# Kernel optimization log

Hardware: AMD Instinct MI355X
Metric: run time of the kernel (lower is better)

The kernel has to match this reference:

```python
import jax, jax.numpy as jnp
import numpy as np

HEAD_NUM = 4
EMB = 128
N_NODES = 50000
N_EDGES = 600000


def setup_inputs() -> dict:
    key = jax.random.key(0)
    k1, k2, k3, k4, k5, k6 = jax.random.split(key, 6)
    embeds = jax.random.normal(k1, (N_NODES, EMB), dtype=jnp.float32)
    qW = jax.random.normal(k2, (EMB, EMB), dtype=jnp.float32) * (1.0 / np.sqrt(EMB))
    kW = jax.random.normal(k3, (EMB, EMB), dtype=jnp.float32) * (1.0 / np.sqrt(EMB))
    vW = jax.random.normal(k4, (EMB, EMB), dtype=jnp.float32) * (1.0 / np.sqrt(EMB))
    rows = jax.random.randint(k5, (N_EDGES,), 0, N_NODES, dtype=jnp.int32)
    cols = jax.random.randint(k6, (N_EDGES,), 0, N_NODES, dtype=jnp.int32)
    return {"embeds": embeds, "qW": qW, "kW": kW, "vW": vW,
            "rows": rows, "cols": cols, "n_nodes": N_NODES}


def reference(embeds, qW, kW, vW, rows, cols, n_nodes):
    H = HEAD_NUM
    D = embeds.shape[1]
    Dh = D // H
    rowEmb = embeds[rows]                                   # [E, D] gather
    colEmb = embeds[cols]                                   # [E, D] gather
    q = (rowEmb @ qW).reshape(-1, H, Dh)                    # [E, H, Dh]
    k = (colEmb @ kW).reshape(-1, H, Dh)
    v = (colEmb @ vW).reshape(-1, H, Dh)
    att = jnp.einsum('ehd,ehd->eh', q, k)                   # per-edge per-head logits
    att = jnp.clip(att, -10.0, 10.0)
    expAtt = jnp.exp(att)                                   # [E, H]
    attNorm = jax.ops.segment_sum(expAtt, rows, num_segments=n_nodes)  # [N, H]
    att = expAtt / (attNorm[rows] + 1e-8)                   # segment softmax
    res = (att[..., None] * v).reshape(-1, D)               # [E, D]
    out = jax.ops.segment_sum(res, rows, num_segments=n_nodes)  # [N, D]
    return out
```

## Files before the change

### kernel.cpp

```cpp
#include <hip/hip_runtime.h>
#include <math.h>

#define EMB 128
#define HEADS 4
#define ROWSTRIDE 152
#define OSTRIDE 260
#define CAP 64

typedef __attribute__((ext_vector_type(8))) _Float16 f16x8;
typedef __attribute__((ext_vector_type(4))) _Float16 f16x4;
typedef __attribute__((ext_vector_type(4))) float f32x4;

__global__ __launch_bounds__(256) void prep_w(
    const float* __restrict__ Wq, const float* __restrict__ Wk, const float* __restrict__ Wv,
    _Float16* __restrict__ Wfrag)
{
    int flat = blockIdx.x * 256 + threadIdx.x;
    int m    = flat >> 14;
    int rem  = flat & 16383;
    int ct   = rem >> 11;
    int s    = (rem >> 9) & 3;
    int lane = (rem >> 3) & 63;
    int j    = rem & 7;
    int k = s * 32 + (lane >> 4) * 8 + j;
    int n = ct * 16 + (lane & 15);
    const float* Ws[3] = { Wq, Wk, Wv };
    Wfrag[flat] = (_Float16)Ws[m][k * 128 + n];
}

__global__ __launch_bounds__(256) void mega_kernel(
    const float* __restrict__ embeds,
    const _Float16* __restrict__ Wfrag,
    _Float16* __restrict__ Qh, _Float16* __restrict__ KV,
    const int* __restrict__ rows, const int* __restrict__ cols,
    int* __restrict__ deg, int* __restrict__ slots,
    int N, int E, int PB)
{
    __shared__ __align__(16) _Float16 sBuf[64 * OSTRIDE];

    if (blockIdx.x >= PB) {
        int e = (blockIdx.x - PB) * 256 + threadIdx.x;
        if (e < E) {
            int r = rows[e];
            int pos = atomicAdd(&deg[r], 1);
            if (pos < CAP) slots[(size_t)r * CAP + pos] = cols[e];
        }
        return;
    }

    const int n0 = blockIdx.x * 64;
    const int t  = threadIdx.x;

    #pragma unroll
    for (int j = 0; j < 8; j++) {
        int flat = t + j * 256;
        int row  = flat >> 5;
        int c4   = flat & 31;
        int gn   = n0 + row;
        float4 v = (gn < N) ? reinterpret_cast<const float4*>(embeds)[(size_t)gn * 32 + c4]
                            : make_float4(0.f, 0.f, 0.f, 0.f);
        f16x4 u = { (_Float16)v.x, (_Float16)v.y, (_Float16)v.z, (_Float16)v.w };
        *reinterpret_cast<f16x4*>(&sBuf[row * ROWSTRIDE + c4 * 4]) = u;
    }
    __syncthreads();

    const int w    = t >> 6;
    const int lane = t & 63;
    const int nlo  = lane & 15;
    const int quad = lane >> 4;

    f16x8 a[4];
    #pragma unroll
    for (int s = 0; s < 4; s++) {
        int row = 16 * w + nlo;
        int k   = s * 32 + quad * 8;
        a[s] = *reinterpret_cast<const f16x8*>(&sBuf[row * ROWSTRIDE + k]);
    }
    __syncthreads();

    const int rowL = 16 * w + quad * 4;

    #pragma unroll
    for (int ct = 0; ct < 8; ct++) {
        f32x4 acc = { 0.f, 0.f, 0.f, 0.f };
        #pragma unroll
        for (int s = 0; s < 4; s++) {
            f16x8 b = *reinterpret_cast<const f16x8*>(
                Wfrag + ((size_t)(ct * 4 + s) * 64 + lane) * 8);
            acc = __builtin_amdgcn_mfma_f32_16x16x32_f16(a[s], b, acc, 0, 0, 0);
        }
        int col = ct * 16 + nlo;
        #pragma unroll
        for (int r = 0; r < 4; r++)
            sBuf[(rowL + r) * OSTRIDE + col] = (_Float16)acc[r];
    }
    __syncthreads();
    #pragma unroll
    for (int j = 0; j < 4; j++) {
        int flat = j * 2048 + t * 8;
        int row  = flat >> 7;
        int col  = flat & 127;
        int gn   = n0 + row;
        if (gn < N) {
            f16x8 v = *reinterpret_cast<const f16x8*>(&sBuf[row * OSTRIDE + col]);
            *reinterpret_cast<f16x8*>(&Qh[(size_t)gn * EMB + col]) = v;
        }
    }
    __syncthreads();

    #pragma unroll
    for (int m = 1; m < 3; m++) {
        int voff = (m == 2) ? 4 : 0;
        #pragma unroll
        for (int ct = 0; ct < 8; ct++) {
            f32x4 acc = { 0.f, 0.f, 0.f, 0.f };
            #pragma unroll
            for (int s = 0; s < 4; s++) {
                f16x8 b = *reinterpret_cast<const f16x8*>(
                    Wfrag + ((size_t)((m * 8 + ct) * 4 + s) * 64 + lane) * 8);
                acc = __builtin_amdgcn_mfma_f32_16x16x32_f16(a[s], b, acc, 0, 0, 0);
            }
            int col  = ct * 16 + nlo;
            int lidx = 8 * (col >> 2) + (col & 3) + voff;
            #pragma unroll
            for (int r = 0; r < 4; r++)
                sBuf[(rowL + r) * OSTRIDE + lidx] = (_Float16)acc[r];
        }
    }
    __syncthreads();
    #pragma unroll
    for (int j = 0; j < 8; j++) {
        int flat = j * 2048 + t * 8;
        int row  = flat >> 8;
        int col  = flat & 255;
        int gn   = n0 + row;
        if (gn < N) {
            f16x8 v = *reinterpret_cast<const f16x8*>(&sBuf[row * OSTRIDE + col]);
            *reinterpret_cast<f16x8*>(&KV[(size_t)gn * 256 + col]) = v;
        }
    }
}

__global__ __launch_bounds__(256) void node_fused(
    const _Float16* __restrict__ Qh, const _Float16* __restrict__ KV,
    const int* __restrict__ deg, const int* __restrict__ slots,
    float* __restrict__ out, int N)
{
    int n = blockIdx.x * 8 + (threadIdx.x >> 5);
    if (n >= N) return;
    int lane = threadIdx.x & 31;

    f16x4 qh = *reinterpret_cast<const f16x4*>(Qh + (size_t)n * EMB + lane * 4);
    float qx = (float)qh.x, qy = (float)qh.y, qz = (float)qh.z, qw = (float)qh.w;

    int cnt = deg[n];
    if (cnt > CAP) cnt = CAP;
    const int* sl = slots + (size_t)n * CAP;

    float4 acc = make_float4(0.f, 0.f, 0.f, 0.f);
    float norm = 0.f;

    const _Float16* KVl = KV + 8 * lane;
    int i = 0;

    for (; i + 4 <= cnt; i += 4) {
        int c0 = sl[i], c1 = sl[i + 1], c2 = sl[i + 2], c3 = sl[i + 3];
        f16x8 kv0 = *reinterpret_cast<const f16x8*>(KVl + (size_t)c0 * 256);
        f16x8 kv1 = *reinterpret_cast<const f16x8*>(KVl + (size_t)c1 * 256);
        f16x8 kv2 = *reinterpret_cast<const f16x8*>(KVl + (size_t)c2 * 256);
        f16x8 kv3 = *reinterpret_cast<const f16x8*>(KVl + (size_t)c3 * 256);

        float d0 = qx * (float)kv0[0] + qy * (float)kv0[1] + qz * (float)kv0[2] + qw * (float)kv0[3];
        float d1 = qx * (float)kv1[0] + qy * (float)kv1[1] + qz * (float)kv1[2] + qw * (float)kv1[3];
        float d2 = qx * (float)kv2[0] + qy * (float)kv2[1] + qz * (float)kv2[2] + qw * (float)kv2[3];
        float d3 = qx * (float)kv3[0] + qy * (float)kv3[1] + qz * (float)kv3[2] + qw * (float)kv3[3];
        d0 += __shfl_xor(d0, 1); d1 += __shfl_xor(d1, 1); d2 += __shfl_xor(d2, 1); d3 += __shfl_xor(d3, 1);
        d0 += __shfl_xor(d0, 2); d1 += __shfl_xor(d1, 2); d2 += __shfl_xor(d2, 2); d3 += __shfl_xor(d3, 2);
        d0 += __shfl_xor(d0, 4); d1 += __shfl_xor(d1, 4); d2 += __shfl_xor(d2, 4); d3 += __shfl_xor(d3, 4);

        float ea0 = exp2f(fminf(10.f, fmaxf(-10.f, d0)) * 1.44269504f);
        float ea1 = exp2f(fminf(10.f, fmaxf(-10.f, d1)) * 1.44269504f);
        float ea2 = exp2f(fminf(10.f, fmaxf(-10.f, d2)) * 1.44269504f);
        float ea3 = exp2f(fminf(10.f, fmaxf(-10.f, d3)) * 1.44269504f);

        acc.x = fmaf(ea0, (float)kv0[4], acc.x);
        acc.y = fmaf(ea0, (float)kv0[5], acc.y);
        acc.z = fmaf(ea0, (float)kv0[6], acc.z);
        acc.w = fmaf(ea0, (float)kv0[7], acc.w);
        acc.x = fmaf(ea1, (float)kv1[4], acc.x);
        acc.y = fmaf(ea1, (float)kv1[5], acc.y);
        acc.z = fmaf(ea1, (float)kv1[6], acc.z);
        acc.w = fmaf(ea1, (float)kv1[7], acc.w);
        acc.x = fmaf(ea2, (float)kv2[4], acc.x);
        acc.y = fmaf(ea2, (float)kv2[5], acc.y);
        acc.z = fmaf(ea2, (float)kv2[6], acc.z);
        acc.w = fmaf(ea2, (float)kv2[7], acc.w);
        acc.x = fmaf(ea3, (float)kv3[4], acc.x);
        acc.y = fmaf(ea3, (float)kv3[5], acc.y);
        acc.z = fmaf(ea3, (float)kv3[6], acc.z);
        acc.w = fmaf(ea3, (float)kv3[7], acc.w);
        norm += ea0 + ea1 + ea2 + ea3;
    }
    for (; i < cnt; i++) {
        int c0 = sl[i];
        f16x8 kv0 = *reinterpret_cast<const f16x8*>(KVl + (size_t)c0 * 256);
        float d0 = qx * (float)kv0[0] + qy * (float)kv0[1] + qz * (float)kv0[2] + qw * (float)kv0[3];
        d0 += __shfl_xor(d0, 1);
        d0 += __shfl_xor(d0, 2);
        d0 += __shfl_xor(d0, 4);
        float ea0 = exp2f(fminf(10.f, fmaxf(-10.f, d0)) * 1.44269504f);
        acc.x = fmaf(ea0, (float)kv0[4], acc.x);
        acc.y = fmaf(ea0, (float)kv0[5], acc.y);
        acc.z = fmaf(ea0, (float)kv0[6], acc.z);
        acc.w = fmaf(ea0, (float)kv0[7], acc.w);
        norm += ea0;
    }

    float inv = 1.f / (norm + 1e-8f);
    acc.x *= inv; acc.y *= inv; acc.z *= inv; acc.w *= inv;
    reinterpret_cast<float4*>(out + (size_t)n * EMB)[lane] = acc;
}

extern "C" void kernel_launch(void* const* d_in, const int* in_sizes, int n_in,
                              void* d_out, int out_size, void* d_ws, size_t ws_size,
                              hipStream_t stream) {
    const float* embeds = (const float*)d_in[0];
    const float* qW     = (const float*)d_in[1];
    const float* kW     = (const float*)d_in[2];
    const float* vW     = (const float*)d_in[3];
    const int*   rows   = (const int*)d_in[4];
    const int*   cols   = (const int*)d_in[5];

    const int N = in_sizes[0] / EMB;
    const int E = in_sizes[4];

    _Float16*  Qh    = (_Float16*)d_ws;
    _Float16*  KV    = Qh + (size_t)N * EMB;
    _Float16*  Wfrag = KV + (size_t)N * 256;
    int*       deg   = (int*)(Wfrag + 3 * 16384);
    int*       slots = deg + N;

    float* out = (float*)d_out;

    (void)hipMemsetAsync(deg, 0, (size_t)N * sizeof(int), stream);

    prep_w<<<192, 256, 0, stream>>>(qW, kW, vW, Wfrag);

    const int PB = (N + 63) / 64;
    const int FB = (E + 255) / 256;
    mega_kernel<<<PB + FB, 256, 0, stream>>>(embeds, Wfrag, Qh, KV,
                                             rows, cols, deg, slots, N, E, PB);

    node_fused<<<(N + 7) / 8, 256, 0, stream>>>(Qh, KV, deg, slots, out, N);
}
```

Before: 179.4 us.

## Swap MFMA operands to write Q/K/V directly from registers, fuse memset

The projection kernel now computes the transposed product (weights as A, embeddings as B), so each lane holds four consecutive output columns of one node. This lets it write Q and interleaved K/V straight to global memory without staging through shared memory and the extra barriers. Q, K and V are computed together in one loop over column tiles. Q is now stored in fp32, which doubles Q traffic but removes a conversion in the consumer. The deg memset is folded into the weight-prep kernel to save an API call and a launch.

```diff
diff --git a/kernel.cpp b/kernel.cpp
--- a/kernel.cpp
+++ b/kernel.cpp
@@ -2,41 +2,44 @@
 #include <math.h>
 
 #define EMB 128
-#define HEADS 4
 #define ROWSTRIDE 152
-#define OSTRIDE 260
 #define CAP 64
 
 typedef __attribute__((ext_vector_type(8))) _Float16 f16x8;
 typedef __attribute__((ext_vector_type(4))) _Float16 f16x4;
 typedef __attribute__((ext_vector_type(4))) float f32x4;
 
-__global__ __launch_bounds__(256) void prep_w(
+__global__ __launch_bounds__(256) void prep_and_zero(
     const float* __restrict__ Wq, const float* __restrict__ Wk, const float* __restrict__ Wv,
-    _Float16* __restrict__ Wfrag)
+    _Float16* __restrict__ Wfrag, int* __restrict__ deg, int N)
 {
-    int flat = blockIdx.x * 256 + threadIdx.x;
-    int m    = flat >> 14;
-    int rem  = flat & 16383;
-    int ct   = rem >> 11;
-    int s    = (rem >> 9) & 3;
-    int lane = (rem >> 3) & 63;
-    int j    = rem & 7;
-    int k = s * 32 + (lane >> 4) * 8 + j;
-    int n = ct * 16 + (lane & 15);
-    const float* Ws[3] = { Wq, Wk, Wv };
-    Wfrag[flat] = (_Float16)Ws[m][k * 128 + n];
+    if (blockIdx.x < 192) {
+        int flat = blockIdx.x * 256 + threadIdx.x;
+        int m    = flat >> 14;
+        int rem  = flat & 16383;
+        int ct   = rem >> 11;
+        int s    = (rem >> 9) & 3;
+        int lane = (rem >> 3) & 63;
+        int j    = rem & 7;
+        int k = s * 32 + (lane >> 4) * 8 + j;
+        int n = ct * 16 + (lane & 15);
+        const float* Ws[3] = { Wq, Wk, Wv };
+        Wfrag[flat] = (_Float16)Ws[m][k * 128 + n];
+    } else {
+        int i = (blockIdx.x - 192) * 256 + threadIdx.x;
+        if (i < N) deg[i] = 0;
+    }
 }
 
 __global__ __launch_bounds__(256) void mega_kernel(
     const float* __restrict__ embeds,
     const _Float16* __restrict__ Wfrag,
-    _Float16* __restrict__ Qh, _Float16* __restrict__ KV,
+    float* __restrict__ Q, _Float16* __restrict__ KV,
     const int* __restrict__ rows, const int* __restrict__ cols,
     int* __restrict__ deg, int* __restrict__ slots,
     int N, int E, int PB)
 {
-    __shared__ __align__(16) _Float16 sBuf[64 * OSTRIDE];
+    __shared__ __align__(16) _Float16 sA[64 * ROWSTRIDE];
 
     if (blockIdx.x >= PB) {
         int e = (blockIdx.x - PB) * 256 + threadIdx.x;
@@ -60,7 +63,7 @@
         float4 v = (gn < N) ? reinterpret_cast<const float4*>(embeds)[(size_t)gn * 32 + c4]
                             : make_float4(0.f, 0.f, 0.f, 0.f);
         f16x4 u = { (_Float16)v.x, (_Float16)v.y, (_Float16)v.z, (_Float16)v.w };
-        *reinterpret_cast<f16x4*>(&sBuf[row * ROWSTRIDE + c4 * 4]) = u;
+        *reinterpret_cast<f16x4*>(&sA[row * ROWSTRIDE + c4 * 4]) = u;
     }
     __syncthreads();
 
@@ -74,75 +77,45 @@
     for (int s = 0; s < 4; s++) {
         int row = 16 * w + nlo;
         int k   = s * 32 + quad * 8;
-        a[s] = *reinterpret_cast<const f16x8*>(&sBuf[row * ROWSTRIDE + k]);
-    }
-    __syncthreads();
-
-    const int rowL = 16 * w + quad * 4;
+        a[s] = *reinterpret_cast<const f16x8*>(&sA[row * ROWSTRIDE + k]);
+    }
+
+    const int node = n0 + 16 * w + nlo;
+    const bool ok  = (node < N);
 
     #pragma unroll
     for (int ct = 0; ct < 8; ct++) {
-        f32x4 acc = { 0.f, 0.f, 0.f, 0.f };
+        f32x4 aq = { 0.f, 0.f, 0.f, 0.f };
+        f32x4 ak = { 0.f, 0.f, 0.f, 0.f };
+        f32x4 av = { 0.f, 0.f, 0.f, 0.f };
         #pragma unroll
         for (int s = 0; s < 4; s++) {
-            f16x8 b = *reinterpret_cast<const f16x8*>(
-                Wfrag + ((size_t)(ct * 4 + s) * 64 + lane) * 8);
-            acc = __builtin_amdgcn_mfma_f32_16x16x32_f16(a[s], b, acc, 0, 0, 0);
+            f16x8 bq = *reinterpret_cast<const f16x8*>(
+                Wfrag + ((size_t)((0 * 8 + ct) * 4 + s) * 64 + lane) * 8);
+            f16x8 bk = *reinterpret_cast<const f16x8*>(
+                Wfrag + ((size_t)((1 * 8 + ct) * 4 + s) * 64 + lane) * 8);
+            f16x8 bv = *reinterpret_cast<const f16x8*>(
+                Wfrag + ((size_t)((2 * 8 + ct) * 4 + s) * 64 + lane) * 8);
+            aq = __builtin_amdgcn_mfma_f32_16x16x32_f16(bq, a[s], aq, 0, 0, 0);
+            ak = __builtin_amdgcn_mfma_f32_16x16x32_f16(bk, a[s], ak, 0, 0, 0);
+            av = __builtin_amdgcn_mfma_f32_16x16x32_f16(bv, a[s], av, 0, 0, 0);
         }
-        int col = ct * 16 + nlo;
-        #pragma unroll
-        for (int r = 0; r < 4; r++)
-            sBuf[(rowL + r) * OSTRIDE + col] = (_Float16)acc[r];
-    }
-    __syncthreads();
-    #pragma unroll
-    for (int j = 0; j < 4; j++) {
-        int flat = j * 2048 + t * 8;
-        int row  = flat >> 7;
-        int col  = flat & 127;
-        int gn   = n0 + row;
-        if (gn < N) {
-            f16x8 v = *reinterpret_cast<const f16x8*>(&sBuf[row * OSTRIDE + col]);
-            *reinterpret_cast<f16x8*>(&Qh[(size_t)gn * EMB + col]) = v;
+        if (ok) {
+            float4 q4 = make_float4(aq[0], aq[1], aq[2], aq[3]);
+            *reinterpret_cast<float4*>(Q + (size_t)node * EMB + ct * 16 + quad * 4) = q4;
+            f16x8 kv;
+            #pragma unroll
+            for (int r = 0; r < 4; r++) {
+                kv[r]     = (_Float16)ak[r];
+                kv[4 + r] = (_Float16)av[r];
+            }
+            *reinterpret_cast<f16x8*>(KV + (size_t)node * 256 + (ct * 4 + quad) * 8) = kv;
         }
     }
-    __syncthreads();
-
-    #pragma unroll
-    for (int m = 1; m < 3; m++) {
-        int voff = (m == 2) ? 4 : 0;
-        #pragma unroll
-        for (int ct = 0; ct < 8; ct++) {
-            f32x4 acc = { 0.f, 0.f, 0.f, 0.f };
-            #pragma unroll
-            for (int s = 0; s < 4; s++) {
-                f16x8 b = *reinterpret_cast<const f16x8*>(
-                    Wfrag + ((size_t)((m * 8 + ct) * 4 + s) * 64 + lane) * 8);
-                acc = __builtin_amdgcn_mfma_f32_16x16x32_f16(a[s], b, acc, 0, 0, 0);
-            }
-            int col  = ct * 16 + nlo;
-            int lidx = 8 * (col >> 2) + (col & 3) + voff;
-            #pragma unroll
-            for (int r = 0; r < 4; r++)
-                sBuf[(rowL + r) * OSTRIDE + lidx] = (_Float16)acc[r];
-        }
-    }
-    __syncthreads();
-    #pragma unroll
-    for (int j = 0; j < 8; j++) {
-        int flat = j * 2048 + t * 8;
-        int row  = flat >> 8;
-        int col  = flat & 255;
-        int gn   = n0 + row;
-        if (gn < N) {
-            f16x8 v = *reinterpret_cast<const f16x8*>(&sBuf[row * OSTRIDE + col]);
-            *reinterpret_cast<f16x8*>(&KV[(size_t)gn * 256 + col]) = v;
-        }
-    }
 }
 
 __global__ __launch_bounds__(256) void node_fused(
-    const _Float16* __restrict__ Qh, const _Float16* __restrict__ KV,
+    const float* __restrict__ Q, const _Float16* __restrict__ KV,
     const int* __restrict__ deg, const int* __restrict__ slots,
     float* __restrict__ out, int N)
 {
@@ -150,8 +123,8 @@
     if (n >= N) return;
     int lane = threadIdx.x & 31;
 
-    f16x4 qh = *reinterpret_cast<const f16x4*>(Qh + (size_t)n * EMB + lane * 4);
-    float qx = (float)qh.x, qy = (float)qh.y, qz = (float)qh.z, qw = (float)qh.w;
+    float4 q4 = reinterpret_cast<const float4*>(Q + (size_t)n * EMB)[lane];
+    float qx = q4.x, qy = q4.y, qz = q4.z, qw = q4.w;
 
     int cnt = deg[n];
     if (cnt > CAP) cnt = CAP;
@@ -234,22 +207,21 @@
     const int N = in_sizes[0] / EMB;
     const int E = in_sizes[4];
 
-    _Float16*  Qh    = (_Float16*)d_ws;
-    _Float16*  KV    = Qh + (size_t)N * EMB;
+    float*     Q     = (float*)d_ws;
+    _Float16*  KV    = (_Float16*)(Q + (size_t)N * EMB);
     _Float16*  Wfrag = KV + (size_t)N * 256;
     int*       deg   = (int*)(Wfrag + 3 * 16384);
     int*       slots = deg + N;
 
     float* out = (float*)d_out;
 
-    (void)hipMemsetAsync(deg, 0, (size_t)N * sizeof(int), stream);
-
-    prep_w<<<192, 256, 0, stream>>>(qW, kW, vW, Wfrag);
+    const int ZB = (N + 255) / 256;
+    prep_and_zero<<<192 + ZB, 256, 0, stream>>>(qW, kW, vW, Wfrag, deg, N);
 
     const int PB = (N + 63) / 64;
     const int FB = (E + 255) / 256;
-    mega_kernel<<<PB + FB, 256, 0, stream>>>(embeds, Wfrag, Qh, KV,
+    mega_kernel<<<PB + FB, 256, 0, stream>>>(embeds, Wfrag, Q, KV,
                                              rows, cols, deg, slots, N, E, PB);
 
-    node_fused<<<(N + 7) / 8, 256, 0, stream>>>(Qh, KV, deg, slots, out, N);
-}
+    node_fused<<<(N + 7) / 8, 256, 0, stream>>>(Q, KV, deg, slots, out, N);
+}
```

Result: slower. 184.1 us (+2.6%).
